# Kernel optimization log

Measured on AMD Instinct MI355X. Metric: run time of the kernel, lower is better.

## Reference

```python
import jax, jax.numpy as jnp
import numpy as np

NHEADS = 8
HD = 64          # h_emb_dim = embed_dim // num_heads
IN_EMB_LEN = 5   # agent-aware: k_same, k_other, q_same, q_other, v
PAD = 1          # kernel_size // 2


def conv2d(x, w, b):
    y = jax.lax.conv_general_dilated(
        x, w, window_strides=(1, 1), padding=[(PAD, PAD), (PAD, PAD)],
        dimension_numbers=("NCHW", "OIHW", "NCHW"))
    return y + b[None, :, None, None]


def setup_inputs() -> dict:
    key = jax.random.key(0)
    ks = jax.random.split(key, 6)
    b, seq, c, h, w = 1, 384, 512, 8, 8
    inp = jax.random.normal(ks[0], (b, seq, c, h, w), dtype=jnp.float32)
    attn_mask = jax.random.normal(ks[1], (b * NHEADS, seq, seq), dtype=jnp.float32) * 0.1
    agent_aware_mask = jax.random.randint(ks[2], (b * NHEADS, seq, seq), 0, 2, dtype=jnp.int32)
    w_in = jax.random.normal(ks[3], (IN_EMB_LEN * c, c, 3, 3), dtype=jnp.float32) * 0.02
    b_in = jnp.zeros((IN_EMB_LEN * c,), dtype=jnp.float32)
    w_out = jax.random.normal(ks[4], (c, c, 3, 3), dtype=jnp.float32) * 0.02
    b_out = jnp.zeros((c,), dtype=jnp.float32)
    return {"inp": inp, "attn_mask": attn_mask, "agent_aware_mask": agent_aware_mask,
            "w_in": w_in, "b_in": b_in, "w_out": w_out, "b_out": b_out}


def reference(inp, attn_mask, agent_aware_mask, w_in, b_in, w_out, b_out):
    b, seq, c, h, w = inp.shape
    hw = h * w
    x = inp.reshape(b * seq, c, h, w)
    feats = conv2d(x, w_in, b_in)                      # [b*seq, 5*c, h, w]
    feats = feats.reshape(b, seq, IN_EMB_LEN * HD, NHEADS * hw)
    feats = jnp.transpose(feats, (0, 3, 1, 2)).reshape(b * NHEADS, hw, seq, IN_EMB_LEN * HD)
    k_same, k_other, q_same, q_other, v = jnp.split(feats, IN_EMB_LEN, axis=3)
    scale = 1.0 / jnp.sqrt(jnp.asarray(HD, dtype=feats.dtype))
    am = attn_mask[:, None]                            # [b*H, 1, seq, seq]
    s_same = jnp.einsum("bpqd,bpkd->bpqk", q_same * scale, k_same) + am
    s_other = jnp.einsum("bpqd,bpkd->bpqk", q_other * scale, k_other) + am
    a_same = jax.nn.softmax(s_same, axis=-1)
    a_other = jax.nn.softmax(s_other, axis=-1)
    m = agent_aware_mask.astype(feats.dtype)[:, None]  # [b*H, 1, seq, seq]
    attn = m * a_same + (1.0 - m) * a_other
    out = jnp.einsum("bpqk,bpkd->bpqd", attn, v)       # [b*H, hw, seq, HD]
    out = out.reshape(b, NHEADS * hw, seq, HD)
    out = jnp.transpose(out, (0, 2, 3, 1)).reshape(b * seq, c, h, w)
    out = conv2d(out, w_out, b_out)
    return out.reshape(b, seq, c, h, w)
```

## Files before the change

kernel.cpp:

```cpp
#include <hip/hip_runtime.h>
#include <stdint.h>
#include <stddef.h>

typedef __attribute__((ext_vector_type(4))) float floatx4;
typedef __attribute__((ext_vector_type(8))) short shortx8;
typedef __attribute__((ext_vector_type(4))) short shortx4;

#define DEVI static __device__ __forceinline__

DEVI uint16_t f2bf(float f) {
  uint32_t u = __builtin_bit_cast(uint32_t, f);
  u += 0x7fffu + ((u >> 16) & 1u);
  return (uint16_t)(u >> 16);
}

DEVI void gload_lds16(const void* g, void* lds) {
  unsigned int off = (unsigned int)(uintptr_t)lds;
  __builtin_amdgcn_global_load_lds(
      (const __attribute__((address_space(1))) unsigned int*)g,
      (__attribute__((address_space(3))) unsigned int*)off,
      16, 0, 0);
}


__global__ __launch_bounds__(256) void k_prep_x(const float* __restrict__ inp,
                                                uint16_t* __restrict__ Xb) {
  int gid = blockIdx.x * 256 + threadIdx.x;
  int ci = gid & 511;
  int ts = gid >> 9;
  int s = ts & 63, t = ts >> 6;
  Xb[gid] = f2bf(inp[((size_t)t * 512 + ci) * 64 + s]);
}

__global__ __launch_bounds__(256) void k_prep_win(const float* __restrict__ w_in,
                                                  const float* __restrict__ b_in,
                                                  uint16_t* __restrict__ Wr,
                                                  float* __restrict__ bias_p) {
  int gid = blockIdx.x * 256 + threadIdx.x;
  int ci = gid & 511;
  int rest = gid >> 9;
  int cp = rest % 2560;
  int tap = rest / 2560;
  int e = cp >> 9, h = (cp >> 6) & 7, d = cp & 63;
  int co = e * 512 + d * 8 + h;
  Wr[gid] = f2bf(w_in[(size_t)co * 4608 + ci * 9 + tap]);
  if (gid < 2560) {
    int e2 = gid >> 9, h2 = (gid >> 6) & 7, d2 = gid & 63;
    bias_p[gid] = b_in[e2 * 512 + d2 * 8 + h2];
  }
}

__global__ __launch_bounds__(256) void k_prep_wout(const float* __restrict__ w_out,
                                                   uint16_t* __restrict__ Wr) {
  int gid = blockIdx.x * 256 + threadIdx.x;
  int c2p = gid & 511;
  int rest = gid >> 9;
  int co2 = rest & 511;
  int tap = rest >> 9;
  int oci = (c2p & 63) * 8 + (c2p >> 6);
  Wr[gid] = f2bf(w_out[(size_t)co2 * 4608 + oci * 9 + tap]);
}

template <int MTOT, int EPI>
__global__ __launch_bounds__(256) void conv_gemm(const uint16_t* __restrict__ W,
                                                 const uint16_t* __restrict__ X,
                                                 const float* __restrict__ bias,
                                                 uint16_t* __restrict__ Fo,
                                                 float* __restrict__ Oo) {
  __shared__ __attribute__((aligned(16))) uint16_t Wl[128 * 64];
  __shared__ __attribute__((aligned(16))) uint16_t Xl[128 * 64];

  const int tid = threadIdx.x;
  const int lane = tid & 63;
  const int wave = tid >> 6;
  const int quad = lane >> 4;
  const int l15 = lane & 15;
  const int wm = wave >> 1;
  const int wn = wave & 1;

  const int m_blk = blockIdx.x / 192;
  const int n_blk = blockIdx.x % 192;
  const int m0 = m_blk * 128;
  const long n0 = (long)n_blk * 128;

  const int srow = wave * 32 + (lane >> 3);
  const int spos = lane & 7;

  floatx4 acc[4][4];
#pragma unroll
  for (int i = 0; i < 4; ++i)
#pragma unroll
    for (int j = 0; j < 4; ++j) acc[i][j] = (floatx4)0.0f;

  int arow[4];
#pragma unroll
  for (int mt = 0; mt < 4; ++mt) arow[mt] = wm * 64 + mt * 16 + l15;

  for (int kc = 0; kc < 8; ++kc) {
    for (int tap = 0; tap < 9; ++tap) {
      __syncthreads();
      if (tap == 0) {
#pragma unroll
        for (int i = 0; i < 4; ++i) {
          int row = srow + i * 8;
          int c = spos ^ (row & 7);
          gload_lds16(X + ((n0 + row) * 512 + kc * 64 + c * 8),
                      Xl + row * 64 + spos * 8);
        }
      }
      {
        const uint16_t* wg = W + ((size_t)tap * MTOT + m0) * 512 + kc * 64;
#pragma unroll
        for (int i = 0; i < 4; ++i) {
          int row = srow + i * 8;
          int c = spos ^ (row & 7);
          gload_lds16(wg + (size_t)row * 512 + c * 8, Wl + row * 64 + spos * 8);
        }
      }
      __syncthreads();

      const int dy = tap / 3 - 1, dx = tap % 3 - 1;
      int brow[4];
      bool bok[4];
#pragma unroll
      for (int nt = 0; nt < 4; ++nt) {
        int s = nt * 16 + l15;
        int y = (s >> 3) + dy, x = (s & 7) + dx;
        bool ok = ((unsigned)y < 8u) && ((unsigned)x < 8u);
        bok[nt] = ok;
        brow[nt] = wn * 64 + (ok ? (y * 8 + x) : 0);
      }

#pragma unroll
      for (int ks = 0; ks < 2; ++ks) {
        shortx8 af[4], bf[4];
#pragma unroll
        for (int mt = 0; mt < 4; ++mt) {
          int pos = ((ks << 2) | quad) ^ (arow[mt] & 7);
          af[mt] = *(const shortx8*)(Wl + arow[mt] * 64 + pos * 8);
        }
#pragma unroll
        for (int nt = 0; nt < 4; ++nt) {
          int pos = ((ks << 2) | quad) ^ (brow[nt] & 7);
          shortx8 v = *(const shortx8*)(Xl + brow[nt] * 64 + pos * 8);
          bf[nt] = bok[nt] ? v : (shortx8)(short)0;
        }
#pragma unroll
        for (int mt = 0; mt < 4; ++mt)
#pragma unroll
          for (int nt = 0; nt < 4; ++nt)
            acc[mt][nt] = __builtin_amdgcn_mfma_f32_16x16x32_bf16(
                af[mt], bf[nt], acc[mt][nt], 0, 0, 0);
      }
    }
  }

  if (EPI == 0) {
#pragma unroll
    for (int mt = 0; mt < 4; ++mt) {
      int cpb = m0 + wm * 64 + mt * 16 + quad * 4;
      floatx4 bv = *(const floatx4*)(bias + cpb);
      int e = cpb >> 9, h = (cpb >> 6) & 7, d0 = cpb & 63;
#pragma unroll
      for (int nt = 0; nt < 4; ++nt) {
        long ng = n0 + wn * 64 + nt * 16 + l15;
        int t = (int)(ng >> 6), p = (int)(ng & 63);
        shortx4 pk;
#pragma unroll
        for (int r = 0; r < 4; ++r) pk[r] = (short)f2bf(acc[mt][nt][r] + bv[r]);
        *(shortx4*)(Fo + ((((size_t)(e * 8 + h) * 64 + p) * 384 + t) * 64 + d0)) = pk;
      }
    }
  } else {
#pragma unroll
    for (int mt = 0; mt < 4; ++mt) {
      int co = m0 + wm * 64 + mt * 16 + quad * 4;
      floatx4 bv = *(const floatx4*)(bias + co);
#pragma unroll
      for (int nt = 0; nt < 4; ++nt) {
        long ng = n0 + wn * 64 + nt * 16 + l15;
        int t = (int)(ng >> 6), s = (int)(ng & 63);
        float* op = Oo + ((size_t)t * 512 + co) * 64 + s;
#pragma unroll
        for (int r = 0; r < 4; ++r) op[(size_t)r * 64] = acc[mt][nt][r] + bv[r];
      }
    }
  }
}

__global__ __launch_bounds__(256) void attn_kernel(const uint16_t* __restrict__ F,
                                                   const float* __restrict__ amask,
                                                   const int* __restrict__ gmask,
                                                   uint16_t* __restrict__ G) {
  __shared__ __attribute__((aligned(16))) uint16_t Vt[64 * 88];
  __shared__ __attribute__((aligned(16))) uint16_t Pl[4][16 * 88];

  const int tid = threadIdx.x;
  const int lane = tid & 63;
  const int wave = tid >> 6;
  const int quad = lane >> 4;
  const int l15 = lane & 15;

  const int qt = blockIdx.x % 6;
  const int hp = blockIdx.x / 6;
  const int h = hp >> 6, p = hp & 63;

  const size_t slab = (size_t)384 * 64;
  const uint16_t* Ks = F + ((size_t)(0 * 8 + h) * 64 + p) * slab;
  const uint16_t* Ko = F + ((size_t)(1 * 8 + h) * 64 + p) * slab;
  const uint16_t* Qs = F + ((size_t)(2 * 8 + h) * 64 + p) * slab;
  const uint16_t* Qo = F + ((size_t)(3 * 8 + h) * 64 + p) * slab;
  const uint16_t* Vv = F + ((size_t)(4 * 8 + h) * 64 + p) * slab;

  const int q0 = qt * 64 + wave * 16;

  shortx8 qsf[2], qof[2];
#pragma unroll
  for (int ks = 0; ks < 2; ++ks) {
    qsf[ks] = *(const shortx8*)(Qs + (size_t)(q0 + l15) * 64 + ks * 32 + quad * 8);
    qof[ks] = *(const shortx8*)(Qo + (size_t)(q0 + l15) * 64 + ks * 32 + quad * 8);
  }

  floatx4 Os[4], Oo4[4];
#pragma unroll
  for (int i = 0; i < 4; ++i) { Os[i] = (floatx4)0.0f; Oo4[i] = (floatx4)0.0f; }
  float ms[4], mo[4], ls[4], lo[4];
#pragma unroll
  for (int r = 0; r < 4; ++r) { ms[r] = -1e30f; mo[r] = -1e30f; ls[r] = 0.f; lo[r] = 0.f; }

  const float SC = 0.125f;
  const float L2E = 1.44269504f;

  const int vk = tid & 63;
  const int vdc = tid >> 6;

  for (int kb = 0; kb < 6; ++kb) {
    const int k0 = kb * 64;
    __syncthreads();
    {
      const uint16_t* vg = Vv + (size_t)(k0 + vk) * 64 + vdc * 16;
      shortx8 v0 = *(const shortx8*)(vg);
      shortx8 v1 = *(const shortx8*)(vg + 8);
#pragma unroll
      for (int e = 0; e < 8; ++e) Vt[(vdc * 16 + e) * 88 + vk] = (uint16_t)v0[e];
#pragma unroll
      for (int e = 0; e < 8; ++e) Vt[(vdc * 16 + 8 + e) * 88 + vk] = (uint16_t)v1[e];
    }
    __syncthreads();

    floatx4 Ssm[4], Sot[4];
#pragma unroll
    for (int nt = 0; nt < 4; ++nt) { Ssm[nt] = (floatx4)0.0f; Sot[nt] = (floatx4)0.0f; }
#pragma unroll
    for (int nt = 0; nt < 4; ++nt) {
      const size_t krow = (size_t)(k0 + nt * 16 + l15) * 64;
#pragma unroll
      for (int ks = 0; ks < 2; ++ks) {
        shortx8 kf = *(const shortx8*)(Ks + krow + ks * 32 + quad * 8);
        Ssm[nt] = __builtin_amdgcn_mfma_f32_16x16x32_bf16(qsf[ks], kf, Ssm[nt], 0, 0, 0);
        shortx8 kf2 = *(const shortx8*)(Ko + krow + ks * 32 + quad * 8);
        Sot[nt] = __builtin_amdgcn_mfma_f32_16x16x32_bf16(qof[ks], kf2, Sot[nt], 0, 0, 0);
      }
    }

    const float* amr = amask + ((size_t)h * 384 + (q0 + quad * 4)) * 384 + k0 + l15;
    const int* gmr = gmask + ((size_t)h * 384 + (q0 + quad * 4)) * 384 + k0 + l15;
    float am[4][4], gm[4][4];
#pragma unroll
    for (int r = 0; r < 4; ++r)
#pragma unroll
      for (int nt = 0; nt < 4; ++nt) {
        am[r][nt] = amr[(size_t)r * 384 + nt * 16];
        gm[r][nt] = (float)gmr[(size_t)r * 384 + nt * 16];
      }
#pragma unroll
    for (int nt = 0; nt < 4; ++nt)
#pragma unroll
      for (int r = 0; r < 4; ++r) {
        Ssm[nt][r] = Ssm[nt][r] * SC + am[r][nt];
        Sot[nt][r] = Sot[nt][r] * SC + am[r][nt];
      }

    float Ps[4][4], Po[4][4];
#pragma unroll
    for (int r = 0; r < 4; ++r) {
      float mx = fmaxf(fmaxf(Ssm[0][r], Ssm[1][r]), fmaxf(Ssm[2][r], Ssm[3][r]));
#pragma unroll
      for (int off = 1; off < 16; off <<= 1) mx = fmaxf(mx, __shfl_xor(mx, off, 16));
      float nm = fmaxf(ms[r], mx);
      float al = exp2f((ms[r] - nm) * L2E);
      ms[r] = nm;
      float rs = 0.f;
#pragma unroll
      for (int nt = 0; nt < 4; ++nt) {
        float pe = exp2f((Ssm[nt][r] - nm) * L2E);
        Ps[nt][r] = pe; rs += pe;
      }
#pragma unroll
      for (int off = 1; off < 16; off <<= 1) rs += __shfl_xor(rs, off, 16);
      ls[r] = ls[r] * al + rs;
#pragma unroll
      for (int nt = 0; nt < 4; ++nt) Os[nt][r] *= al;
      float mx2 = fmaxf(fmaxf(Sot[0][r], Sot[1][r]), fmaxf(Sot[2][r], Sot[3][r]));
#pragma unroll
      for (int off = 1; off < 16; off <<= 1) mx2 = fmaxf(mx2, __shfl_xor(mx2, off, 16));
      float nm2 = fmaxf(mo[r], mx2);
      float al2 = exp2f((mo[r] - nm2) * L2E);
      mo[r] = nm2;
      float rs2 = 0.f;
#pragma unroll
      for (int nt = 0; nt < 4; ++nt) {
        float pe = exp2f((Sot[nt][r] - nm2) * L2E);
        Po[nt][r] = pe; rs2 += pe;
      }
#pragma unroll
      for (int off = 1; off < 16; off <<= 1) rs2 += __shfl_xor(rs2, off, 16);
      lo[r] = lo[r] * al2 + rs2;
#pragma unroll
      for (int nt = 0; nt < 4; ++nt) Oo4[nt][r] *= al2;
    }

    uint16_t* myP = &Pl[wave][0];
#pragma unroll
    for (int nt = 0; nt < 4; ++nt)
#pragma unroll
      for (int r = 0; r < 4; ++r)
        myP[(quad * 4 + r) * 88 + nt * 16 + l15] = f2bf(Ps[nt][r] * gm[r][nt]);
    shortx8 pa[2];
#pragma unroll
    for (int ks = 0; ks < 2; ++ks)
      pa[ks] = *(const shortx8*)(myP + l15 * 88 + ks * 32 + quad * 8);
#pragma unroll
    for (int nt = 0; nt < 4; ++nt)
#pragma unroll
      for (int ks = 0; ks < 2; ++ks) {
        shortx8 vb = *(const shortx8*)(Vt + (nt * 16 + l15) * 88 + ks * 32 + quad * 8);
        Os[nt] = __builtin_amdgcn_mfma_f32_16x16x32_bf16(pa[ks], vb, Os[nt], 0, 0, 0);
      }
#pragma unroll
    for (int nt = 0; nt < 4; ++nt)
#pragma unroll
      for (int r = 0; r < 4; ++r)
        myP[(quad * 4 + r) * 88 + nt * 16 + l15] = f2bf(Po[nt][r] * (1.f - gm[r][nt]));
#pragma unroll
    for (int ks = 0; ks < 2; ++ks)
      pa[ks] = *(const shortx8*)(myP + l15 * 88 + ks * 32 + quad * 8);
#pragma unroll
    for (int nt = 0; nt < 4; ++nt)
#pragma unroll
      for (int ks = 0; ks < 2; ++ks) {
        shortx8 vb = *(const shortx8*)(Vt + (nt * 16 + l15) * 88 + ks * 32 + quad * 8);
        Oo4[nt] = __builtin_amdgcn_mfma_f32_16x16x32_bf16(pa[ks], vb, Oo4[nt], 0, 0, 0);
      }
  }

#pragma unroll
  for (int r = 0; r < 4; ++r) { ls[r] = 1.f / ls[r]; lo[r] = 1.f / lo[r]; }
#pragma unroll
  for (int nt = 0; nt < 4; ++nt) {
    int d = nt * 16 + l15;
#pragma unroll
    for (int r = 0; r < 4; ++r) {
      int t = q0 + quad * 4 + r;
      G[((size_t)t * 64 + p) * 512 + h * 64 + d] = f2bf(Os[nt][r] * ls[r] + Oo4[nt][r] * lo[r]);
    }
  }
}


extern "C" void kernel_launch(void* const* d_in, const int* in_sizes, int n_in,
                              void* d_out, int out_size, void* d_ws, size_t ws_size,
                              hipStream_t stream) {
  (void)in_sizes; (void)n_in; (void)out_size;

  const float* inp   = (const float*)d_in[0];
  const float* amask = (const float*)d_in[1];
  const int*   gmask = (const int*)d_in[2];
  const float* w_in  = (const float*)d_in[3];
  const float* b_in  = (const float*)d_in[4];
  const float* w_out = (const float*)d_in[5];
  const float* b_out = (const float*)d_in[6];
  float* out = (float*)d_out;

  const size_t SZ_WRIN  = (size_t)9 * 2560 * 512 * 2;
  const size_t SZ_WROUT = (size_t)9 * 512 * 512 * 2;
  const size_t SZ_BIAS  = 2560 * 4;
  const size_t SZ_XB    = (size_t)24576 * 512 * 2;
  const size_t SZ_F     = (size_t)5 * 8 * 64 * 384 * 64 * 2;
  if (ws_size < SZ_WRIN + SZ_WROUT + SZ_BIAS + SZ_XB + SZ_F) return;

  char* ws = (char*)d_ws;
  uint16_t* Wr_in  = (uint16_t*)ws;  ws += SZ_WRIN;
  uint16_t* Wr_out = (uint16_t*)ws;  ws += SZ_WROUT;
  float*    bias_p = (float*)ws;     ws += SZ_BIAS;
  uint16_t* Xb     = (uint16_t*)ws;  ws += SZ_XB;
  uint16_t* F      = (uint16_t*)ws;  ws += SZ_F;
  uint16_t* G      = Xb;

  k_prep_x<<<49152, 256, 0, stream>>>(inp, Xb);
  k_prep_win<<<46080, 256, 0, stream>>>(w_in, b_in, Wr_in, bias_p);
  k_prep_wout<<<9216, 256, 0, stream>>>(w_out, Wr_out);
  conv_gemm<2560, 0><<<20 * 192, 256, 0, stream>>>(Wr_in, Xb, bias_p, F, nullptr);
  attn_kernel<<<512 * 6, 256, 0, stream>>>(F, amask, gmask, G);
  conv_gemm<512, 1><<<4 * 192, 256, 0, stream>>>(Wr_out, G, b_out, nullptr, out);
}
```

Baseline: 1.221 ms.

## Tile-transpose prep kernels, pre-transpose masks, and restructure attention to transposed-score MFMA

Rewrites the input and weight prep kernels to transpose through shared memory with vectorized loads and stores instead of one strided gather per element. Adds a kernel that transposes the attention and agent masks once (pre-scaling by log2e) into the now-free weight buffer. The attention kernel computes transposed scores (K·Q), so the softmax reduction runs across lanes with fewer shuffles and P stays in registers as fp16 MFMA operands without an LDS round-trip. V is staged once per block as fp16 instead of per key block, which removes most per-iteration barriers. Converting V and P to fp16 changes precision, and reusing the Wr_in buffer adds an ordering dependency on the first conv.

```diff
diff --git a/kernel.cpp b/kernel.cpp
--- a/kernel.cpp
+++ b/kernel.cpp
@@ -5,6 +5,7 @@
 typedef __attribute__((ext_vector_type(4))) float floatx4;
 typedef __attribute__((ext_vector_type(8))) short shortx8;
 typedef __attribute__((ext_vector_type(4))) short shortx4;
+typedef __attribute__((ext_vector_type(4))) _Float16 halfx4;
 
 #define DEVI static __device__ __forceinline__
 
@@ -12,6 +13,9 @@
   uint32_t u = __builtin_bit_cast(uint32_t, f);
   u += 0x7fffu + ((u >> 16) & 1u);
   return (uint16_t)(u >> 16);
+}
+DEVI float bf2f(uint16_t u) {
+  return __builtin_bit_cast(float, (uint32_t)u << 16);
 }
 
 DEVI void gload_lds16(const void* g, void* lds) {
@@ -25,40 +29,134 @@
 
 __global__ __launch_bounds__(256) void k_prep_x(const float* __restrict__ inp,
                                                 uint16_t* __restrict__ Xb) {
-  int gid = blockIdx.x * 256 + threadIdx.x;
-  int ci = gid & 511;
-  int ts = gid >> 9;
-  int s = ts & 63, t = ts >> 6;
-  Xb[gid] = f2bf(inp[((size_t)t * 512 + ci) * 64 + s]);
+  __shared__ float T[64 * 65];
+  const int tid = threadIdx.x;
+  const int t = blockIdx.x >> 3, cb = blockIdx.x & 7;
+  const float* src = inp + ((size_t)t * 512 + cb * 64) * 64;
+  {
+    int ci = tid >> 2, so = (tid & 3) * 16;
+#pragma unroll
+    for (int j = 0; j < 4; ++j) {
+      float4 v = *(const float4*)&src[ci * 64 + so + 4 * j];
+      T[ci * 65 + so + 4 * j + 0] = v.x;
+      T[ci * 65 + so + 4 * j + 1] = v.y;
+      T[ci * 65 + so + 4 * j + 2] = v.z;
+      T[ci * 65 + so + 4 * j + 3] = v.w;
+    }
+  }
+  __syncthreads();
+  {
+    int s = tid >> 2, co = (tid & 3) * 16;
+    uint16_t* dst = Xb + ((size_t)(t * 64 + s) * 512) + cb * 64 + co;
+    shortx8 o0, o1;
+#pragma unroll
+    for (int j = 0; j < 8; ++j) o0[j] = (short)f2bf(T[(co + j) * 65 + s]);
+#pragma unroll
+    for (int j = 0; j < 8; ++j) o1[j] = (short)f2bf(T[(co + 8 + j) * 65 + s]);
+    *(shortx8*)dst = o0;
+    *(shortx8*)(dst + 8) = o1;
+  }
 }
 
 __global__ __launch_bounds__(256) void k_prep_win(const float* __restrict__ w_in,
                                                   const float* __restrict__ b_in,
                                                   uint16_t* __restrict__ Wr,
                                                   float* __restrict__ bias_p) {
-  int gid = blockIdx.x * 256 + threadIdx.x;
-  int ci = gid & 511;
-  int rest = gid >> 9;
-  int cp = rest % 2560;
-  int tap = rest / 2560;
-  int e = cp >> 9, h = (cp >> 6) & 7, d = cp & 63;
-  int co = e * 512 + d * 8 + h;
-  Wr[gid] = f2bf(w_in[(size_t)co * 4608 + ci * 9 + tap]);
-  if (gid < 2560) {
-    int e2 = gid >> 9, h2 = (gid >> 6) & 7, d2 = gid & 63;
-    bias_p[gid] = b_in[e2 * 512 + d2 * 8 + h2];
+  __shared__ float B[4608];
+  const int tid = threadIdx.x;
+  const int cp = blockIdx.x;
+  const int e = cp >> 9, h = (cp >> 6) & 7, d = cp & 63;
+  const int co = e * 512 + d * 8 + h;
+  const float* src = w_in + (size_t)co * 4608;
+#pragma unroll
+  for (int it = 0; it < 9; ++it) {
+    int i2 = it * 256 + tid;
+    *(float2*)&B[i2 * 2] = *(const float2*)&src[i2 * 2];
+  }
+  if (tid == 0) bias_p[cp] = b_in[co];
+  __syncthreads();
+  const int ci = tid * 2;
+#pragma unroll
+  for (int tap = 0; tap < 9; ++tap) {
+    uint32_t pk = (uint32_t)f2bf(B[ci * 9 + tap]) |
+                  ((uint32_t)f2bf(B[(ci + 1) * 9 + tap]) << 16);
+    *(uint32_t*)&Wr[((size_t)tap * 2560 + cp) * 512 + ci] = pk;
   }
 }
 
 __global__ __launch_bounds__(256) void k_prep_wout(const float* __restrict__ w_out,
                                                    uint16_t* __restrict__ Wr) {
-  int gid = blockIdx.x * 256 + threadIdx.x;
-  int c2p = gid & 511;
-  int rest = gid >> 9;
-  int co2 = rest & 511;
-  int tap = rest >> 9;
-  int oci = (c2p & 63) * 8 + (c2p >> 6);
-  Wr[gid] = f2bf(w_out[(size_t)co2 * 4608 + oci * 9 + tap]);
+  __shared__ float B[4608];
+  const int tid = threadIdx.x;
+  const int co2 = blockIdx.x;
+  const float* src = w_out + (size_t)co2 * 4608;
+#pragma unroll
+  for (int it = 0; it < 9; ++it) {
+    int i2 = it * 256 + tid;
+    *(float2*)&B[i2 * 2] = *(const float2*)&src[i2 * 2];
+  }
+  __syncthreads();
+  const int c2 = tid * 2;
+  const int oci0 = (c2 & 63) * 8 + (c2 >> 6);
+  const int oci1 = ((c2 + 1) & 63) * 8 + ((c2 + 1) >> 6);
+#pragma unroll
+  for (int tap = 0; tap < 9; ++tap) {
+    uint32_t pk = (uint32_t)f2bf(B[oci0 * 9 + tap]) |
+                  ((uint32_t)f2bf(B[oci1 * 9 + tap]) << 16);
+    *(uint32_t*)&Wr[((size_t)tap * 512 + co2) * 512 + c2] = pk;
+  }
+}
+
+__global__ __launch_bounds__(256) void k_prep_mask(const float* __restrict__ am,
+                                                   const int* __restrict__ gm,
+                                                   float* __restrict__ amT,
+                                                   float* __restrict__ gmT) {
+  __shared__ float A_[64 * 65];
+  __shared__ float G_[64 * 65];
+  const int tid = threadIdx.x;
+  const int b = blockIdx.x;
+  const int h = b / 36, rr = b % 36;
+  const int q0 = (rr / 6) * 64, k0 = (rr % 6) * 64;
+  {
+    int qr = tid >> 2, ko = (tid & 3) * 16;
+    const float* ap = am + ((size_t)h * 384 + q0 + qr) * 384 + k0 + ko;
+    const int* gp = gm + ((size_t)h * 384 + q0 + qr) * 384 + k0 + ko;
+#pragma unroll
+    for (int j = 0; j < 4; ++j) {
+      float4 v = *(const float4*)(ap + 4 * j);
+      int4 g = *(const int4*)(gp + 4 * j);
+      int kk = ko + 4 * j;
+      A_[(kk + 0) * 65 + qr] = v.x;
+      A_[(kk + 1) * 65 + qr] = v.y;
+      A_[(kk + 2) * 65 + qr] = v.z;
+      A_[(kk + 3) * 65 + qr] = v.w;
+      G_[(kk + 0) * 65 + qr] = (float)g.x;
+      G_[(kk + 1) * 65 + qr] = (float)g.y;
+      G_[(kk + 2) * 65 + qr] = (float)g.z;
+      G_[(kk + 3) * 65 + qr] = (float)g.w;
+    }
+  }
+  __syncthreads();
+  {
+    const float L2E = 1.44269504f;
+    int kr = tid >> 2, qo = (tid & 3) * 16;
+    float* aop = amT + ((size_t)h * 384 + k0 + kr) * 384 + q0 + qo;
+    float* gop = gmT + ((size_t)h * 384 + k0 + kr) * 384 + q0 + qo;
+#pragma unroll
+    for (int j = 0; j < 4; ++j) {
+      float4 o, g;
+      o.x = A_[kr * 65 + qo + 4 * j + 0] * L2E;
+      o.y = A_[kr * 65 + qo + 4 * j + 1] * L2E;
+      o.z = A_[kr * 65 + qo + 4 * j + 2] * L2E;
+      o.w = A_[kr * 65 + qo + 4 * j + 3] * L2E;
+      g.x = G_[kr * 65 + qo + 4 * j + 0];
+      g.y = G_[kr * 65 + qo + 4 * j + 1];
+      g.z = G_[kr * 65 + qo + 4 * j + 2];
+      g.w = G_[kr * 65 + qo + 4 * j + 3];
+      *(float4*)(aop + 4 * j) = o;
+      *(float4*)(gop + 4 * j) = g;
+    }
+  }
 }
 
 template <int MTOT, int EPI>
@@ -189,11 +287,10 @@
 }
 
 __global__ __launch_bounds__(256) void attn_kernel(const uint16_t* __restrict__ F,
-                                                   const float* __restrict__ amask,
-                                                   const int* __restrict__ gmask,
+                                                   const float* __restrict__ amT,
+                                                   const float* __restrict__ gmT,
                                                    uint16_t* __restrict__ G) {
-  __shared__ __attribute__((aligned(16))) uint16_t Vt[64 * 88];
-  __shared__ __attribute__((aligned(16))) uint16_t Pl[4][16 * 88];
+  __shared__ __attribute__((aligned(16))) _Float16 Vt[64 * 392];
 
   const int tid = threadIdx.x;
   const int lane = tid & 63;
@@ -212,8 +309,25 @@
   const uint16_t* Qo = F + ((size_t)(3 * 8 + h) * 64 + p) * slab;
   const uint16_t* Vv = F + ((size_t)(4 * 8 + h) * 64 + p) * slab;
 
+  if (tid < 192) {
+    const int kk0 = tid * 2;
+    const uint16_t* v0 = Vv + (size_t)kk0 * 64;
+#pragma unroll
+    for (int dc = 0; dc < 8; ++dc) {
+      shortx8 a = *(const shortx8*)(v0 + dc * 8);
+      shortx8 b = *(const shortx8*)(v0 + 64 + dc * 8);
+#pragma unroll
+      for (int e = 0; e < 8; ++e) {
+        _Float16 fa = (_Float16)bf2f((uint16_t)a[e]);
+        _Float16 fb = (_Float16)bf2f((uint16_t)b[e]);
+        uint32_t pk = (uint32_t)__builtin_bit_cast(uint16_t, fa) |
+                      ((uint32_t)__builtin_bit_cast(uint16_t, fb) << 16);
+        *(uint32_t*)&Vt[(dc * 8 + e) * 392 + kk0] = pk;
+      }
+    }
+  }
+
   const int q0 = qt * 64 + wave * 16;
-
   shortx8 qsf[2], qof[2];
 #pragma unroll
   for (int ks = 0; ks < 2; ++ks) {
@@ -221,149 +335,133 @@
     qof[ks] = *(const shortx8*)(Qo + (size_t)(q0 + l15) * 64 + ks * 32 + quad * 8);
   }
 
-  floatx4 Os[4], Oo4[4];
-#pragma unroll
-  for (int i = 0; i < 4; ++i) { Os[i] = (floatx4)0.0f; Oo4[i] = (floatx4)0.0f; }
-  float ms[4], mo[4], ls[4], lo[4];
-#pragma unroll
-  for (int r = 0; r < 4; ++r) { ms[r] = -1e30f; mo[r] = -1e30f; ls[r] = 0.f; lo[r] = 0.f; }
-
-  const float SC = 0.125f;
-  const float L2E = 1.44269504f;
-
-  const int vk = tid & 63;
-  const int vdc = tid >> 6;
+  floatx4 Os[4], Oo[4];
+#pragma unroll
+  for (int i = 0; i < 4; ++i) { Os[i] = (floatx4)0.0f; Oo[i] = (floatx4)0.0f; }
+  float ms = -1e30f, mo = -1e30f, ls = 0.f, lo = 0.f;
+
+  const float C1 = 0.125f * 1.44269504f;
+
+  __syncthreads();
 
   for (int kb = 0; kb < 6; ++kb) {
     const int k0 = kb * 64;
-    __syncthreads();
-    {
-      const uint16_t* vg = Vv + (size_t)(k0 + vk) * 64 + vdc * 16;
-      shortx8 v0 = *(const shortx8*)(vg);
-      shortx8 v1 = *(const shortx8*)(vg + 8);
-#pragma unroll
-      for (int e = 0; e < 8; ++e) Vt[(vdc * 16 + e) * 88 + vk] = (uint16_t)v0[e];
-#pragma unroll
-      for (int e = 0; e < 8; ++e) Vt[(vdc * 16 + 8 + e) * 88 + vk] = (uint16_t)v1[e];
-    }
-    __syncthreads();
-
-    floatx4 Ssm[4], Sot[4];
-#pragma unroll
-    for (int nt = 0; nt < 4; ++nt) { Ssm[nt] = (floatx4)0.0f; Sot[nt] = (floatx4)0.0f; }
+
+    const float* amr = amT + ((size_t)h * 384 + k0 + quad * 4) * 384 + q0 + l15;
+    float am[4][4];
+#pragma unroll
+    for (int nt = 0; nt < 4; ++nt)
+#pragma unroll
+      for (int r = 0; r < 4; ++r) am[nt][r] = amr[((size_t)nt * 16 + r) * 384];
+
+    floatx4 Ss[4], So[4];
+#pragma unroll
+    for (int nt = 0; nt < 4; ++nt) { Ss[nt] = (floatx4)0.0f; So[nt] = (floatx4)0.0f; }
 #pragma unroll
     for (int nt = 0; nt < 4; ++nt) {
       const size_t krow = (size_t)(k0 + nt * 16 + l15) * 64;
 #pragma unroll
       for (int ks = 0; ks < 2; ++ks) {
-        shortx8 kf = *(const shortx8*)(Ks + krow + ks * 32 + quad * 8);
-        Ssm[nt] = __builtin_amdgcn_mfma_f32_16x16x32_bf16(qsf[ks], kf, Ssm[nt], 0, 0, 0);
-        shortx8 kf2 = *(const shortx8*)(Ko + krow + ks * 32 + quad * 8);
-        Sot[nt] = __builtin_amdgcn_mfma_f32_16x16x32_bf16(qof[ks], kf2, Sot[nt], 0, 0, 0);
-      }
-    }
-
-    const float* amr = amask + ((size_t)h * 384 + (q0 + quad * 4)) * 384 + k0 + l15;
-    const int* gmr = gmask + ((size_t)h * 384 + (q0 + quad * 4)) * 384 + k0 + l15;
-    float am[4][4], gm[4][4];
-#pragma unroll
-    for (int r = 0; r < 4; ++r)
-#pragma unroll
-      for (int nt = 0; nt < 4; ++nt) {
-        am[r][nt] = amr[(size_t)r * 384 + nt * 16];
-        gm[r][nt] = (float)gmr[(size_t)r * 384 + nt * 16];
-      }
+        shortx8 ka = *(const shortx8*)(Ks + krow + ks * 32 + quad * 8);
+        Ss[nt] = __builtin_amdgcn_mfma_f32_16x16x32_bf16(ka, qsf[ks], Ss[nt], 0, 0, 0);
+        shortx8 kb_ = *(const shortx8*)(Ko + krow + ks * 32 + quad * 8);
+        So[nt] = __builtin_amdgcn_mfma_f32_16x16x32_bf16(kb_, qof[ks], So[nt], 0, 0, 0);
+      }
+    }
+
+    float Ps[4][4], Po[4][4];
 #pragma unroll
     for (int nt = 0; nt < 4; ++nt)
 #pragma unroll
       for (int r = 0; r < 4; ++r) {
-        Ssm[nt][r] = Ssm[nt][r] * SC + am[r][nt];
-        Sot[nt][r] = Sot[nt][r] * SC + am[r][nt];
-      }
-
-    float Ps[4][4], Po[4][4];
-#pragma unroll
-    for (int r = 0; r < 4; ++r) {
-      float mx = fmaxf(fmaxf(Ssm[0][r], Ssm[1][r]), fmaxf(Ssm[2][r], Ssm[3][r]));
-#pragma unroll
-      for (int off = 1; off < 16; off <<= 1) mx = fmaxf(mx, __shfl_xor(mx, off, 16));
-      float nm = fmaxf(ms[r], mx);
-      float al = exp2f((ms[r] - nm) * L2E);
-      ms[r] = nm;
+        Ps[nt][r] = Ss[nt][r] * C1 + am[nt][r];
+        Po[nt][r] = So[nt][r] * C1 + am[nt][r];
+      }
+
+    {
+      float mx = Ps[0][0];
+#pragma unroll
+      for (int nt = 0; nt < 4; ++nt)
+#pragma unroll
+        for (int r = 0; r < 4; ++r) mx = fmaxf(mx, Ps[nt][r]);
+      mx = fmaxf(mx, __shfl_xor(mx, 16));
+      mx = fmaxf(mx, __shfl_xor(mx, 32));
+      float nm = fmaxf(ms, mx);
+      float al = exp2f(ms - nm);
+      ms = nm;
       float rs = 0.f;
 #pragma unroll
-      for (int nt = 0; nt < 4; ++nt) {
-        float pe = exp2f((Ssm[nt][r] - nm) * L2E);
-        Ps[nt][r] = pe; rs += pe;
-      }
-#pragma unroll
-      for (int off = 1; off < 16; off <<= 1) rs += __shfl_xor(rs, off, 16);
-      ls[r] = ls[r] * al + rs;
-#pragma unroll
-      for (int nt = 0; nt < 4; ++nt) Os[nt][r] *= al;
-      float mx2 = fmaxf(fmaxf(Sot[0][r], Sot[1][r]), fmaxf(Sot[2][r], Sot[3][r]));
-#pragma unroll
-      for (int off = 1; off < 16; off <<= 1) mx2 = fmaxf(mx2, __shfl_xor(mx2, off, 16));
-      float nm2 = fmaxf(mo[r], mx2);
-      float al2 = exp2f((mo[r] - nm2) * L2E);
-      mo[r] = nm2;
-      float rs2 = 0.f;
-#pragma unroll
-      for (int nt = 0; nt < 4; ++nt) {
-        float pe = exp2f((Sot[nt][r] - nm2) * L2E);
-        Po[nt][r] = pe; rs2 += pe;
-      }
-#pragma unroll
-      for (int off = 1; off < 16; off <<= 1) rs2 += __shfl_xor(rs2, off, 16);
-      lo[r] = lo[r] * al2 + rs2;
-#pragma unroll
-      for (int nt = 0; nt < 4; ++nt) Oo4[nt][r] *= al2;
-    }
-
-    uint16_t* myP = &Pl[wave][0];
-#pragma unroll
-    for (int nt = 0; nt < 4; ++nt)
-#pragma unroll
-      for (int r = 0; r < 4; ++r)
-        myP[(quad * 4 + r) * 88 + nt * 16 + l15] = f2bf(Ps[nt][r] * gm[r][nt]);
-    shortx8 pa[2];
-#pragma unroll
-    for (int ks = 0; ks < 2; ++ks)
-      pa[ks] = *(const shortx8*)(myP + l15 * 88 + ks * 32 + quad * 8);
-#pragma unroll
-    for (int nt = 0; nt < 4; ++nt)
-#pragma unroll
-      for (int ks = 0; ks < 2; ++ks) {
-        shortx8 vb = *(const shortx8*)(Vt + (nt * 16 + l15) * 88 + ks * 32 + quad * 8);
-        Os[nt] = __builtin_amdgcn_mfma_f32_16x16x32_bf16(pa[ks], vb, Os[nt], 0, 0, 0);
-      }
-#pragma unroll
-    for (int nt = 0; nt < 4; ++nt)
-#pragma unroll
-      for (int r = 0; r < 4; ++r)
-        myP[(quad * 4 + r) * 88 + nt * 16 + l15] = f2bf(Po[nt][r] * (1.f - gm[r][nt]));
-#pragma unroll
-    for (int ks = 0; ks < 2; ++ks)
-      pa[ks] = *(const shortx8*)(myP + l15 * 88 + ks * 32 + quad * 8);
-#pragma unroll
-    for (int nt = 0; nt < 4; ++nt)
-#pragma unroll
-      for (int ks = 0; ks < 2; ++ks) {
-        shortx8 vb = *(const shortx8*)(Vt + (nt * 16 + l15) * 88 + ks * 32 + quad * 8);
-        Oo4[nt] = __builtin_amdgcn_mfma_f32_16x16x32_bf16(pa[ks], vb, Oo4[nt], 0, 0, 0);
-      }
-  }
-
-#pragma unroll
-  for (int r = 0; r < 4; ++r) { ls[r] = 1.f / ls[r]; lo[r] = 1.f / lo[r]; }
-#pragma unroll
-  for (int nt = 0; nt < 4; ++nt) {
-    int d = nt * 16 + l15;
-#pragma unroll
-    for (int r = 0; r < 4; ++r) {
-      int t = q0 + quad * 4 + r;
-      G[((size_t)t * 64 + p) * 512 + h * 64 + d] = f2bf(Os[nt][r] * ls[r] + Oo4[nt][r] * lo[r]);
-    }
+      for (int nt = 0; nt < 4; ++nt)
+#pragma unroll
+        for (int r = 0; r < 4; ++r) {
+          float pe = exp2f(Ps[nt][r] - nm);
+          Ps[nt][r] = pe;
+          rs += pe;
+        }
+      rs += __shfl_xor(rs, 16);
+      rs += __shfl_xor(rs, 32);
+      ls = ls * al + rs;
+#pragma unroll
+      for (int dt = 0; dt < 4; ++dt) Os[dt] = Os[dt] * al;
+    }
+    {
+      float mx = Po[0][0];
+#pragma unroll
+      for (int nt = 0; nt < 4; ++nt)
+#pragma unroll
+        for (int r = 0; r < 4; ++r) mx = fmaxf(mx, Po[nt][r]);
+      mx = fmaxf(mx, __shfl_xor(mx, 16));
+      mx = fmaxf(mx, __shfl_xor(mx, 32));
+      float nm = fmaxf(mo, mx);
+      float al = exp2f(mo - nm);
+      mo = nm;
+      float rs = 0.f;
+#pragma unroll
+      for (int nt = 0; nt < 4; ++nt)
+#pragma unroll
+        for (int r = 0; r < 4; ++r) {
+          float pe = exp2f(Po[nt][r] - nm);
+          Po[nt][r] = pe;
+          rs += pe;
+        }
+      rs += __shfl_xor(rs, 16);
+      rs += __shfl_xor(rs, 32);
+      lo = lo * al + rs;
+#pragma unroll
+      for (int dt = 0; dt < 4; ++dt) Oo[dt] = Oo[dt] * al;
+    }
+
+    const float* gmr = gmT + ((size_t)h * 384 + k0 + quad * 4) * 384 + q0 + l15;
+    halfx4 pbs[4], pbo[4];
+#pragma unroll
+    for (int kt = 0; kt < 4; ++kt)
+#pragma unroll
+      for (int r = 0; r < 4; ++r) {
+        float g = gmr[((size_t)kt * 16 + r) * 384];
+        pbs[kt][r] = (_Float16)(Ps[kt][r] * g);
+        pbo[kt][r] = (_Float16)(Po[kt][r] * (1.f - g));
+      }
+
+#pragma unroll
+    for (int dt = 0; dt < 4; ++dt) {
+      const _Float16* vrow = Vt + (size_t)(dt * 16 + l15) * 392 + k0;
+#pragma unroll
+      for (int kt = 0; kt < 4; ++kt) {
+        halfx4 va = *(const halfx4*)(vrow + kt * 16 + quad * 4);
+        Os[dt] = __builtin_amdgcn_mfma_f32_16x16x16f16(va, pbs[kt], Os[dt], 0, 0, 0);
+        Oo[dt] = __builtin_amdgcn_mfma_f32_16x16x16f16(va, pbo[kt], Oo[dt], 0, 0, 0);
+      }
+    }
+  }
+
+  const float is = 1.f / ls, io = 1.f / lo;
+  const int q = q0 + l15;
+#pragma unroll
+  for (int dt = 0; dt < 4; ++dt) {
+    shortx4 pk;
+#pragma unroll
+    for (int r = 0; r < 4; ++r) pk[r] = (short)f2bf(Os[dt][r] * is + Oo[dt][r] * io);
+    *(shortx4*)(G + ((size_t)q * 64 + p) * 512 + h * 64 + dt * 16 + quad * 4) = pk;
   }
 }
 
@@ -396,11 +494,14 @@
   uint16_t* Xb     = (uint16_t*)ws;  ws += SZ_XB;
   uint16_t* F      = (uint16_t*)ws;  ws += SZ_F;
   uint16_t* G      = Xb;
-
-  k_prep_x<<<49152, 256, 0, stream>>>(inp, Xb);
-  k_prep_win<<<46080, 256, 0, stream>>>(w_in, b_in, Wr_in, bias_p);
-  k_prep_wout<<<9216, 256, 0, stream>>>(w_out, Wr_out);
+  float*    amT    = (float*)Wr_in;
+  float*    gmT    = amT + (size_t)8 * 384 * 384;
+
+  k_prep_x<<<3072, 256, 0, stream>>>(inp, Xb);
+  k_prep_win<<<2560, 256, 0, stream>>>(w_in, b_in, Wr_in, bias_p);
+  k_prep_wout<<<512, 256, 0, stream>>>(w_out, Wr_out);
   conv_gemm<2560, 0><<<20 * 192, 256, 0, stream>>>(Wr_in, Xb, bias_p, F, nullptr);
-  attn_kernel<<<512 * 6, 256, 0, stream>>>(F, amask, gmask, G);
+  k_prep_mask<<<288, 256, 0, stream>>>(amask, gmask, amT, gmT);
+  attn_kernel<<<512 * 6, 256, 0, stream>>>(F, amT, gmT, G);
   conv_gemm<512, 1><<<4 * 192, 256, 0, stream>>>(Wr_out, G, b_out, nullptr, out);
 }
```

Result: faster. 1.111 ms (-9.0%).
